# Performance work log

Measured on AMD Instinct MI355X. Metric: run time of the kernel, lower is better.

## Reference

```python
import jax, jax.numpy as jnp
import numpy as np

NB, D, H, DH, DHID = 12, 512, 8, 64, 1024  # n_blocks, d_model, n_heads, d_head, d_hidden
B, S = 2, 2048
EPS = 1e-5


def _ln(x, g, b):
    m = jnp.mean(x, axis=-1, keepdims=True)
    v = jnp.mean(jnp.square(x - m), axis=-1, keepdims=True)
    return (x - m) / jnp.sqrt(v + EPS) * g + b


def setup_inputs() -> dict:
    key = jax.random.key(0)
    ks = jax.random.split(key, 8)
    s = 0.02
    f32 = jnp.float32
    return {
        "X": jax.random.normal(ks[0], (B, S, D), f32),
        "qkv_w": jax.random.normal(ks[1], (NB, D, 3 * D), f32) * s,
        "qkv_b": jnp.zeros((NB, 3 * D), f32),
        "fc_w": jax.random.normal(ks[2], (NB, D, D), f32) * s,
        "fc_b": jnp.zeros((NB, D), f32),
        "ln1_g": jnp.ones((NB, D), f32),
        "ln1_b": jnp.zeros((NB, D), f32),
        "w1": jax.random.normal(ks[3], (NB, D, DHID), f32) * s,
        "b1": jnp.zeros((NB, DHID), f32),
        "w2": jax.random.normal(ks[4], (NB, DHID, D), f32) * s,
        "b2": jnp.zeros((NB, D), f32),
        "ln2_g": jnp.ones((NB, D), f32),
        "ln2_b": jnp.zeros((NB, D), f32),
    }


def reference(X, qkv_w, qkv_b, fc_w, fc_b, ln1_g, ln1_b, w1, b1, w2, b2, ln2_g, ln2_b):
    scale = 1.0 / np.sqrt(D)  # NOTE: original scales by 1/sqrt(d_model), not 1/sqrt(d_head)

    def body(x, p):
        qw, qb, fw, fb, g1, be1, w1_, bb1, w2_, bb2, g2, be2 = p
        b, s, _ = x.shape
        # qkv -> [b, h, s, 3*dh]; split per-head AFTER head reshape (as in chunk(dim=-1))
        ctx = (x @ qw + qb).reshape(b, s, H, 3 * DH).transpose(0, 2, 1, 3)
        q, k, v = jnp.split(ctx, 3, axis=-1)  # each [b, h, s, dh]
        attn = jax.nn.softmax(jnp.einsum('bhqd,bhkd->bhqk', q, k) * scale, axis=-1)
        o = jnp.einsum('bhqk,bhkd->bhqd', attn, v).transpose(0, 2, 1, 3).reshape(b, s, D)
        x = x + (o @ fw + fb)                      # residual + attn out proj (dropout=0)
        h = jax.nn.relu(_ln(x, g1, be1) @ w1_ + bb1)
        x = x + (h @ w2_ + bb2)                    # residual + MLP
        return _ln(x, g2, be2), None

    out, _ = jax.lax.scan(
        body, X,
        (qkv_w, qkv_b, fc_w, fc_b, ln1_g, ln1_b, w1, b1, w2, b2, ln2_g, ln2_b))
    return out
```

## Files before the change

kernel.cpp:

```cpp
#include <hip/hip_runtime.h>

typedef unsigned short ushort_t;
typedef __attribute__((ext_vector_type(8))) short bf16x8;
typedef __attribute__((ext_vector_type(4))) float f32x4;
typedef __attribute__((ext_vector_type(4))) unsigned short us4;

#define DEV __device__ __forceinline__

DEV ushort_t f2b(float f) {
    union { float f; unsigned u; } x; x.f = f;
    unsigned r = (x.u + 0x7fffu + ((x.u >> 16) & 1u)) >> 16;
    return (ushort_t)r;
}

DEV float b2f(ushort_t u) {
    union { unsigned u; float f; } x; x.u = ((unsigned)u) << 16;
    return x.f;
}

DEV unsigned cvt_pk_bf16(float lo, float hi) {
    unsigned r;
    asm("v_cvt_pk_bf16_f32 %0, %1, %2" : "=v"(r) : "v"(lo), "v"(hi));
    return r;
}

typedef void __attribute__((address_space(1)))* gp1;
typedef void __attribute__((address_space(3)))* sp3;
DEV void gload_lds16(const void* g, void* l) {
    __builtin_amdgcn_global_load_lds((gp1)g, (sp3)l, 16, 0, 0);
}

__global__ __launch_bounds__(256) void transpose_cvt(
    const float* __restrict__ in, ushort_t* __restrict__ out, int K, int N)
{
    __shared__ float tile[32][33];
    const int nb = blockIdx.z;
    const float* src = in + (size_t)nb * K * N;
    ushort_t* dst = out + (size_t)nb * K * N;
    const int n0 = blockIdx.x * 32, k0 = blockIdx.y * 32;
    const int tx = threadIdx.x & 31, ty = threadIdx.x >> 5;
#pragma unroll
    for (int i = 0; i < 32; i += 8)
        tile[ty + i][tx] = src[(size_t)(k0 + ty + i) * N + n0 + tx];
    __syncthreads();
#pragma unroll
    for (int i = 0; i < 32; i += 8)
        dst[(size_t)(n0 + ty + i) * K + k0 + tx] = f2b(tile[tx][ty + i]);
}

__global__ __launch_bounds__(256) void init_x(
    const float* __restrict__ X, float* __restrict__ xf, ushort_t* __restrict__ xb)
{
    const int i = blockIdx.x * 256 + threadIdx.x;
    const float4 v = ((const float4*)X)[i];
    ((float4*)xf)[i] = v;
    us4 o = { f2b(v.x), f2b(v.y), f2b(v.z), f2b(v.w) };
    ((us4*)xb)[i] = o;
}

enum { EPI_QKV = 0, EPI_RELUB = 2 };

template<int EPI>
__global__ __launch_bounds__(256, 2) void gemm64(
    const ushort_t* __restrict__ A, const ushort_t* __restrict__ Wt,
    const float* __restrict__ bias, ushort_t* __restrict__ Cb,
    ushort_t* __restrict__ Oq, ushort_t* __restrict__ Ok, ushort_t* __restrict__ Ov,
    int M, int N, int K, float qs)
{
    __shared__ __align__(16) ushort_t lA[2][64 * 64];
    __shared__ __align__(16) ushort_t lB[2][128 * 64];
    const int nbm = M >> 6;
    const int bm = blockIdx.x % nbm;
    const int bn = blockIdx.x / nbm;
    const int tid = threadIdx.x, lane = tid & 63, w = tid >> 6;
    const int l15 = lane & 15, l4 = lane >> 4;

    f32x4 acc[4][2];
#pragma unroll
    for (int i = 0; i < 4; i++)
#pragma unroll
        for (int j = 0; j < 2; j++) { f32x4 z = {0.f, 0.f, 0.f, 0.f}; acc[i][j] = z; }

    const int srow = tid >> 3;
    const int sch = tid & 7;
    const int swch = sch ^ (srow & 7);
    const ushort_t* Asrc0 = A  + (size_t)(bm * 64 + srow) * K + swch * 8;
    const ushort_t* Asrc1 = A  + (size_t)(bm * 64 + srow + 32) * K + swch * 8;
    const ushort_t* Bsrc0 = Wt + (size_t)(bn * 128 + srow) * K + swch * 8;
    const ushort_t* Bsrc1 = Wt + (size_t)(bn * 128 + srow + 32) * K + swch * 8;
    const ushort_t* Bsrc2 = Wt + (size_t)(bn * 128 + srow + 64) * K + swch * 8;
    const ushort_t* Bsrc3 = Wt + (size_t)(bn * 128 + srow + 96) * K + swch * 8;
    char* lAc = (char*)lA;
    char* lBc = (char*)lB;

#define GE_STAGE(buf, k0) do {                                            \
        gload_lds16(Asrc0 + (k0), lAc + (buf) * 8192  + w * 1024);        \
        gload_lds16(Asrc1 + (k0), lAc + (buf) * 8192  + 4096 + w * 1024); \
        gload_lds16(Bsrc0 + (k0), lBc + (buf) * 16384 + w * 1024);        \
        gload_lds16(Bsrc1 + (k0), lBc + (buf) * 16384 + 4096 + w * 1024); \
        gload_lds16(Bsrc2 + (k0), lBc + (buf) * 16384 + 8192 + w * 1024); \
        gload_lds16(Bsrc3 + (k0), lBc + (buf) * 16384 + 12288 + w * 1024);\
    } while (0)

    GE_STAGE(0, 0);
    __syncthreads();

    const int nIt = K >> 6;
    int cur = 0;
    for (int it = 0; it < nIt; ++it) {
        if (it + 1 < nIt) GE_STAGE(cur ^ 1, (it + 1) * 64);
#pragma unroll
        for (int ks = 0; ks < 2; ks++) {
            bf16x8 af[4], bfr[2];
#pragma unroll
            for (int i = 0; i < 4; i++) {
                const int row = i * 16 + l15;
                af[i] = *(const bf16x8*)(lAc + cur * 8192 + row * 128 +
                                         (((ks * 4 + l4) ^ (row & 7)) << 4));
            }
#pragma unroll
            for (int j = 0; j < 2; j++) {
                const int row = w * 32 + j * 16 + l15;
                bfr[j] = *(const bf16x8*)(lBc + cur * 16384 + row * 128 +
                                          (((ks * 4 + l4) ^ (row & 7)) << 4));
            }
#pragma unroll
            for (int i = 0; i < 4; i++)
#pragma unroll
                for (int j = 0; j < 2; j++)
                    acc[i][j] = __builtin_amdgcn_mfma_f32_16x16x32_bf16(af[i], bfr[j], acc[i][j], 0, 0, 0);
        }
        __syncthreads();
        cur ^= 1;
    }
#undef GE_STAGE

    const int mbase = bm * 64;
    const int nbase = bn * 128 + w * 32;
#pragma unroll
    for (int j = 0; j < 2; j++) {
        const int nf16 = nbase + j * 16;
        const float bv = bias[nf16 + l15];
        if constexpr (EPI == EPI_QKV) {
            const int head = nf16 / 192;
            const int rem = nf16 - head * 192;
            const int part = rem >> 6;
            const int dh = (rem & 63) + l15;
#pragma unroll
            for (int i = 0; i < 4; i++) {
                const int m0 = mbase + i * 16 + l4 * 4;
                const int b = m0 >> 11, s0 = m0 & 2047;
                if (part == 2) {
                    us4 pv;
#pragma unroll
                    for (int r = 0; r < 4; r++) pv[r] = f2b(acc[i][j][r] + bv);
                    *(us4*)(&Ov[((size_t)(b * 8 + head) * 64 + dh) * 2048 + s0]) = pv;
                } else if (part == 0) {
#pragma unroll
                    for (int r = 0; r < 4; r++)
                        Oq[((size_t)(b * 8 + head) * 2048 + s0 + r) * 64 + dh] =
                            f2b((acc[i][j][r] + bv) * qs);
                } else {
#pragma unroll
                    for (int r = 0; r < 4; r++)
                        Ok[((size_t)(b * 8 + head) * 2048 + s0 + r) * 64 + dh] =
                            f2b(acc[i][j][r] + bv);
                }
            }
        } else {
#pragma unroll
            for (int i = 0; i < 4; i++) {
                const int m0 = mbase + i * 16 + l4 * 4;
#pragma unroll
                for (int r = 0; r < 4; r++) {
                    const size_t idx = (size_t)(m0 + r) * N + nf16 + l15;
                    const float v = acc[i][j][r] + bv;
                    Cb[idx] = f2b(v > 0.f ? v : 0.f);
                }
            }
        }
    }
}

__global__ __launch_bounds__(256, 2) void gemm64_splitk(
    const ushort_t* __restrict__ A, const ushort_t* __restrict__ Wt,
    float* __restrict__ P0, float* __restrict__ P1, int M, int N, int K)
{
    __shared__ __align__(16) ushort_t lA[2][64 * 64];
    __shared__ __align__(16) ushort_t lB[2][128 * 64];
    const int nbm = M >> 6;
    const int nbn = N >> 7;
    int bid = blockIdx.x;
    const int bm = bid % nbm; bid /= nbm;
    const int bn = bid % nbn;
    const int kh = bid / nbn;
    const int Keff = K >> 1;
    const int kbase = kh * Keff;
    const int tid = threadIdx.x, lane = tid & 63, w = tid >> 6;
    const int l15 = lane & 15, l4 = lane >> 4;

    f32x4 acc[4][2];
#pragma unroll
    for (int i = 0; i < 4; i++)
#pragma unroll
        for (int j = 0; j < 2; j++) { f32x4 z = {0.f, 0.f, 0.f, 0.f}; acc[i][j] = z; }

    const int srow = tid >> 3;
    const int sch = tid & 7;
    const int swch = sch ^ (srow & 7);
    const ushort_t* Asrc0 = A  + (size_t)(bm * 64 + srow) * K + kbase + swch * 8;
    const ushort_t* Asrc1 = A  + (size_t)(bm * 64 + srow + 32) * K + kbase + swch * 8;
    const ushort_t* Bsrc0 = Wt + (size_t)(bn * 128 + srow) * K + kbase + swch * 8;
    const ushort_t* Bsrc1 = Wt + (size_t)(bn * 128 + srow + 32) * K + kbase + swch * 8;
    const ushort_t* Bsrc2 = Wt + (size_t)(bn * 128 + srow + 64) * K + kbase + swch * 8;
    const ushort_t* Bsrc3 = Wt + (size_t)(bn * 128 + srow + 96) * K + kbase + swch * 8;
    char* lAc = (char*)lA;
    char* lBc = (char*)lB;

#define GE_STAGE(buf, k0) do {                                            \
        gload_lds16(Asrc0 + (k0), lAc + (buf) * 8192  + w * 1024);        \
        gload_lds16(Asrc1 + (k0), lAc + (buf) * 8192  + 4096 + w * 1024); \
        gload_lds16(Bsrc0 + (k0), lBc + (buf) * 16384 + w * 1024);        \
        gload_lds16(Bsrc1 + (k0), lBc + (buf) * 16384 + 4096 + w * 1024); \
        gload_lds16(Bsrc2 + (k0), lBc + (buf) * 16384 + 8192 + w * 1024); \
        gload_lds16(Bsrc3 + (k0), lBc + (buf) * 16384 + 12288 + w * 1024);\
    } while (0)

    GE_STAGE(0, 0);
    __syncthreads();

    const int nIt = Keff >> 6;
    int cur = 0;
    for (int it = 0; it < nIt; ++it) {
        if (it + 1 < nIt) GE_STAGE(cur ^ 1, (it + 1) * 64);
#pragma unroll
        for (int ks = 0; ks < 2; ks++) {
            bf16x8 af[4], bfr[2];
#pragma unroll
            for (int i = 0; i < 4; i++) {
                const int row = i * 16 + l15;
                af[i] = *(const bf16x8*)(lAc + cur * 8192 + row * 128 +
                                         (((ks * 4 + l4) ^ (row & 7)) << 4));
            }
#pragma unroll
            for (int j = 0; j < 2; j++) {
                const int row = w * 32 + j * 16 + l15;
                bfr[j] = *(const bf16x8*)(lBc + cur * 16384 + row * 128 +
                                          (((ks * 4 + l4) ^ (row & 7)) << 4));
            }
#pragma unroll
            for (int i = 0; i < 4; i++)
#pragma unroll
                for (int j = 0; j < 2; j++)
                    acc[i][j] = __builtin_amdgcn_mfma_f32_16x16x32_bf16(af[i], bfr[j], acc[i][j], 0, 0, 0);
        }
        __syncthreads();
        cur ^= 1;
    }
#undef GE_STAGE

    float* out = kh ? P1 : P0;
    const int mbase = bm * 64;
    const int nbase = bn * 128 + w * 32;
#pragma unroll
    for (int j = 0; j < 2; j++) {
        const int nf16 = nbase + j * 16;
#pragma unroll
        for (int i = 0; i < 4; i++) {
            const int m0 = mbase + i * 16 + l4 * 4;
#pragma unroll
            for (int r = 0; r < 4; r++)
                out[(size_t)(m0 + r) * N + nf16 + l15] = acc[i][j][r];
        }
    }
}

__global__ __launch_bounds__(256, 4) void flash_attn7(
    const ushort_t* __restrict__ Q, const ushort_t* __restrict__ Kg,
    const ushort_t* __restrict__ Vg, ushort_t* __restrict__ Opart,
    float* __restrict__ lbuf)
{
    __shared__ __align__(16) ushort_t lK[2][64 * 64];
    __shared__ __align__(16) ushort_t lV[2][64 * 64];
    __shared__ __align__(16) ushort_t lP[4][32 * 64];

    const int id = blockIdx.x;
    const int rest = id >> 3;
    const int kvh = rest & 1;
    const int qt = (rest >> 1) & 15;
    const int bh = (id & 7) + ((rest >> 5) << 3);
    const int tid = threadIdx.x, lane = tid & 63, w = tid >> 6;
    const int l15 = lane & 15, l4 = lane >> 4;
    const int qrow0 = qt * 128 + w * 32;

    const ushort_t* Qb = Q + ((size_t)bh * 2048 + qrow0) * 64;
    bf16x8 qf[2][2];
#pragma unroll
    for (int qi = 0; qi < 2; qi++)
#pragma unroll
        for (int ks = 0; ks < 2; ks++)
            qf[qi][ks] = *(const bf16x8*)(Qb + (qi * 16 + l15) * 64 + ks * 32 + l4 * 8);

    const ushort_t* Kbase = Kg + (size_t)bh * 2048 * 64;
    const ushort_t* Vbase = Vg + (size_t)bh * 64 * 2048;

    const f32x4 FZ = { 0.f, 0.f, 0.f, 0.f };
    float l_run[2] = { 0.f, 0.f };
    f32x4 oacc[2][4];
#pragma unroll
    for (int qi = 0; qi < 2; qi++)
#pragma unroll
        for (int nd = 0; nd < 4; nd++) oacc[qi][nd] = FZ;

    char* lKc = (char*)lK;
    char* lVc = (char*)lV;
    char* myP = (char*)(lP[w]);

    const int srow8 = lane >> 3;
    const int sch = lane & 7;

#define FA_STAGE(buf, kt) do {                                              \
        const int row0_ = w * 16 + srow8;                                   \
        const int sc0_ = sch ^ (row0_ & 7);                                 \
        gload_lds16(Kbase + (size_t)((kt) * 64 + row0_) * 64 + sc0_ * 8,    \
                    lKc + (buf) * 8192 + w * 2048);                         \
        gload_lds16(Vbase + (size_t)row0_ * 2048 + (kt) * 64 + sc0_ * 8,    \
                    lVc + (buf) * 8192 + w * 2048);                         \
        gload_lds16(Kbase + (size_t)((kt) * 64 + row0_ + 8) * 64 + sc0_ * 8,\
                    lKc + (buf) * 8192 + w * 2048 + 1024);                  \
        gload_lds16(Vbase + (size_t)(row0_ + 8) * 2048 + (kt) * 64 + sc0_ * 8,\
                    lVc + (buf) * 8192 + w * 2048 + 1024);                  \
    } while (0)

#define FA_BODY(CUR, IT) do {                                               \
    if ((IT) < 15) FA_STAGE((CUR) ^ 1, kt0 + (IT) + 1);                     \
    f32x4 sc[2][4];                                                         \
    __builtin_amdgcn_s_setprio(1);                                          \
    _Pragma("unroll")                                                       \
    for (int nf = 0; nf < 4; nf++) {                                        \
        const int krow = nf * 16 + l15;                                     \
        const bf16x8 kf0 = *(const bf16x8*)(lKc + (CUR) * 8192 + krow * 128 + \
                                            ((l4 ^ (krow & 7)) << 4));      \
        const bf16x8 kf1 = *(const bf16x8*)(lKc + (CUR) * 8192 + krow * 128 + \
                                            (((4 + l4) ^ (krow & 7)) << 4)); \
        sc[0][nf] = __builtin_amdgcn_mfma_f32_16x16x32_bf16(kf0, qf[0][0], FZ, 0, 0, 0); \
        sc[1][nf] = __builtin_amdgcn_mfma_f32_16x16x32_bf16(kf0, qf[1][0], FZ, 0, 0, 0); \
        sc[0][nf] = __builtin_amdgcn_mfma_f32_16x16x32_bf16(kf1, qf[0][1], sc[0][nf], 0, 0, 0); \
        sc[1][nf] = __builtin_amdgcn_mfma_f32_16x16x32_bf16(kf1, qf[1][1], sc[1][nf], 0, 0, 0); \
    }                                                                       \
    __builtin_amdgcn_s_setprio(0);                                          \
    _Pragma("unroll")                                                       \
    for (int qi = 0; qi < 2; qi++) {                                        \
        float ps0 = 0.f, ps1 = 0.f;                                         \
        _Pragma("unroll")                                                   \
        for (int nf = 0; nf < 4; nf++) {                                    \
            const float p0 = exp2f(sc[qi][nf][0]);                          \
            const float p1 = exp2f(sc[qi][nf][1]);                          \
            const float p2 = exp2f(sc[qi][nf][2]);                          \
            const float p3 = exp2f(sc[qi][nf][3]);                          \
            sc[qi][nf][0] = p0; sc[qi][nf][1] = p1;                         \
            sc[qi][nf][2] = p2; sc[qi][nf][3] = p3;                         \
            ps0 += p0 + p2; ps1 += p1 + p3;                                 \
        }                                                                   \
        l_run[qi] += ps0 + ps1;                                             \
    }                                                                       \
    const int hh0 = (l15 >> 3) & 1;                                         \
    _Pragma("unroll")                                                       \
    for (int qi = 0; qi < 2; qi++) {                                        \
        char* rp = myP + (qi * 16 + l15) * 128;                             \
        const int swz = (l15 & 7) << 4;                                     \
        _Pragma("unroll")                                                   \
        for (int nf = 0; nf < 4; nf++) {                                    \
            const unsigned pw0 = cvt_pk_bf16(sc[qi][nf][0], sc[qi][nf][1]); \
            const unsigned pw1 = cvt_pk_bf16(sc[qi][nf][2], sc[qi][nf][3]); \
            const unsigned wA = hh0 ? pw1 : pw0;                            \
            const unsigned wB = hh0 ? pw0 : pw1;                            \
            const int cbase = nf * 32 + l4 * 8;                             \
            *(unsigned*)(rp + ((cbase + hh0 * 4) ^ swz)) = wA;              \
            *(unsigned*)(rp + ((cbase + (1 - hh0) * 4) ^ swz)) = wB;        \
        }                                                                   \
    }                                                                       \
    __asm__ volatile("" ::: "memory");                                     \
    bf16x8 pa[2][2];                                                        \
    _Pragma("unroll")                                                       \
    for (int qi = 0; qi < 2; qi++)                                          \
        _Pragma("unroll")                                                   \
        for (int ks = 0; ks < 2; ks++)                                      \
            pa[qi][ks] = *(const bf16x8*)(myP + (qi * 16 + l15) * 128 +     \
                                          ((ks * 64 + l4 * 16) ^ ((l15 & 7) << 4))); \
    __builtin_amdgcn_s_setprio(1);                                          \
    _Pragma("unroll")                                                       \
    for (int ks = 0; ks < 2; ks++)                                          \
        _Pragma("unroll")                                                   \
        for (int nd = 0; nd < 4; nd++) {                                    \
            const int vrow = nd * 16 + l15;                                 \
            const bf16x8 vf = *(const bf16x8*)(lVc + (CUR) * 8192 + vrow * 128 + \
                                               (((ks * 4 + l4) ^ (vrow & 7)) << 4)); \
            oacc[0][nd] = __builtin_amdgcn_mfma_f32_16x16x32_bf16(pa[0][ks], vf, oacc[0][nd], 0, 0, 0); \
            oacc[1][nd] = __builtin_amdgcn_mfma_f32_16x16x32_bf16(pa[1][ks], vf, oacc[1][nd], 0, 0, 0); \
        }                                                                   \
    __builtin_amdgcn_s_setprio(0);                                          \
    __syncthreads();                                                        \
} while (0)

    const int kt0 = kvh * 16;
    FA_STAGE(0, kt0);
    __syncthreads();

    for (int it2 = 0; it2 < 8; ++it2) {
        FA_BODY(0, it2 * 2);
        FA_BODY(1, it2 * 2 + 1);
    }
#undef FA_BODY
#undef FA_STAGE

#pragma unroll
    for (int qi = 0; qi < 2; qi++) {
        l_run[qi] += __shfl_xor(l_run[qi], 16);
        l_run[qi] += __shfl_xor(l_run[qi], 32);
    }
    ushort_t* Op = Opart + ((size_t)(kvh * 16 + bh) * 2048 + qrow0) * 64;
#pragma unroll
    for (int qi = 0; qi < 2; qi++)
#pragma unroll
        for (int r = 0; r < 4; r++)
#pragma unroll
            for (int nd = 0; nd < 4; nd++)
                Op[(size_t)(qi * 16 + l4 * 4 + r) * 64 + nd * 16 + l15] =
                    f2b(oacc[qi][nd][r]);
    if (lane < 32) {
        const int qi = lane >> 4;
        lbuf[(size_t)(kvh * 16 + bh) * 2048 + qrow0 + qi * 16 + (lane & 15)] =
            qi ? l_run[1] : l_run[0];
    }
}

__global__ __launch_bounds__(256) void combine_attn(
    const ushort_t* __restrict__ Opart, const float* __restrict__ lbuf,
    ushort_t* __restrict__ O)
{
    const int gid = blockIdx.x * 256 + threadIdx.x;
    const int d4 = (gid & 15) * 4;
    const int s = (gid >> 4) & 2047;
    const int bh = gid >> 15;
    const us4 a0 = *(const us4*)(Opart + ((size_t)bh * 2048 + s) * 64 + d4);
    const us4 a1 = *(const us4*)(Opart + ((size_t)(16 + bh) * 2048 + s) * 64 + d4);
    const float l0 = lbuf[(size_t)bh * 2048 + s];
    const float l1 = lbuf[(size_t)(16 + bh) * 2048 + s];
    const float inv = 1.f / (l0 + l1);
    us4 out;
#pragma unroll
    for (int r = 0; r < 4; r++)
        out[r] = f2b((b2f(a0[r]) + b2f(a1[r])) * inv);
    const int row = (bh >> 3) * 2048 + s;
    const int col = (bh & 7) * 64 + d4;
    *(us4*)(&O[(size_t)row * 512 + col]) = out;
}

template<int CN>
__global__ __launch_bounds__(256) void ln_fused(
    const float* __restrict__ Xf, const float* __restrict__ P0,
    const float* __restrict__ P1, const float* __restrict__ bias,
    const float* __restrict__ g, const float* __restrict__ beta,
    float* __restrict__ XfOut, ushort_t* __restrict__ Yb, float* __restrict__ Yf)
{
    const int row = blockIdx.x * 4 + (threadIdx.x >> 6);
    const int lane = threadIdx.x & 63;
    const size_t base = (size_t)row * 512;
    float4 x0 = ((const float4*)(Xf + base))[lane];
    float4 x1 = ((const float4*)(Xf + base))[lane + 64];
    const float4 a0 = ((const float4*)(P0 + base))[lane];
    const float4 a1 = ((const float4*)(P0 + base))[lane + 64];
    const float4 c0 = ((const float4*)(P1 + base))[lane];
    const float4 c1 = ((const float4*)(P1 + base))[lane + 64];
    const float4 bb0 = ((const float4*)bias)[lane];
    const float4 bb1 = ((const float4*)bias)[lane + 64];
    x0.x += a0.x + c0.x + bb0.x; x0.y += a0.y + c0.y + bb0.y;
    x0.z += a0.z + c0.z + bb0.z; x0.w += a0.w + c0.w + bb0.w;
    x1.x += a1.x + c1.x + bb1.x; x1.y += a1.y + c1.y + bb1.y;
    x1.z += a1.z + c1.z + bb1.z; x1.w += a1.w + c1.w + bb1.w;

    float s = x0.x + x0.y + x0.z + x0.w + x1.x + x1.y + x1.z + x1.w;
    float s2 = x0.x * x0.x + x0.y * x0.y + x0.z * x0.z + x0.w * x0.w
             + x1.x * x1.x + x1.y * x1.y + x1.z * x1.z + x1.w * x1.w;
#pragma unroll
    for (int m = 1; m < 64; m <<= 1) { s += __shfl_xor(s, m); s2 += __shfl_xor(s2, m); }
    const float mean = s * (1.f / 512.f);
    const float inv = rsqrtf(s2 * (1.f / 512.f) - mean * mean + 1e-5f);
    const float4 g0 = ((const float4*)g)[lane], g1 = ((const float4*)g)[lane + 64];
    const float4 b0 = ((const float4*)beta)[lane], b1 = ((const float4*)beta)[lane + 64];
    float4 y0, y1;
    y0.x = (x0.x - mean) * inv * g0.x + b0.x;
    y0.y = (x0.y - mean) * inv * g0.y + b0.y;
    y0.z = (x0.z - mean) * inv * g0.z + b0.z;
    y0.w = (x0.w - mean) * inv * g0.w + b0.w;
    y1.x = (x1.x - mean) * inv * g1.x + b1.x;
    y1.y = (x1.y - mean) * inv * g1.y + b1.y;
    y1.z = (x1.z - mean) * inv * g1.z + b1.z;
    y1.w = (x1.w - mean) * inv * g1.w + b1.w;
    if constexpr (CN == 0) {
        ((float4*)(XfOut + base))[lane] = x0;
        ((float4*)(XfOut + base))[lane + 64] = x1;
    } else {
        ((float4*)(XfOut + base))[lane] = y0;
        ((float4*)(XfOut + base))[lane + 64] = y1;
        if (Yf) {
            ((float4*)(Yf + base))[lane] = y0;
            ((float4*)(Yf + base))[lane + 64] = y1;
        }
    }
    us4 o0 = { f2b(y0.x), f2b(y0.y), f2b(y0.z), f2b(y0.w) };
    us4 o1 = { f2b(y1.x), f2b(y1.y), f2b(y1.z), f2b(y1.w) };
    ((us4*)(Yb + base))[lane] = o0;
    ((us4*)(Yb + base))[lane + 64] = o1;
}

extern "C" void kernel_launch(void* const* d_in, const int* in_sizes, int n_in,
                              void* d_out, int out_size, void* d_ws, size_t ws_size,
                              hipStream_t stream)
{
    (void)in_sizes; (void)n_in; (void)out_size; (void)ws_size;
    const float* X     = (const float*)d_in[0];
    const float* qkv_w = (const float*)d_in[1];
    const float* qkv_b = (const float*)d_in[2];
    const float* fc_w  = (const float*)d_in[3];
    const float* fc_b  = (const float*)d_in[4];
    const float* ln1_g = (const float*)d_in[5];
    const float* ln1_b = (const float*)d_in[6];
    const float* w1    = (const float*)d_in[7];
    const float* b1    = (const float*)d_in[8];
    const float* w2    = (const float*)d_in[9];
    const float* b2    = (const float*)d_in[10];
    const float* ln2_g = (const float*)d_in[11];
    const float* ln2_b = (const float*)d_in[12];

    char* ws = (char*)d_ws;
    size_t off = 0;
    auto alloc = [&](size_t bytes) -> char* {
        char* p = ws + off;
        off += (bytes + 255) & ~(size_t)255;
        return p;
    };
    ushort_t* qkvw_t = (ushort_t*)alloc(12ull * 1536 * 512 * 2);
    ushort_t* fcw_t  = (ushort_t*)alloc(12ull * 512 * 512 * 2);
    ushort_t* w1_t   = (ushort_t*)alloc(12ull * 512 * 1024 * 2);
    ushort_t* w2_t   = (ushort_t*)alloc(12ull * 1024 * 512 * 2);
    float*    xf     = (float*)   alloc(4096ull * 512 * 4);
    ushort_t* xb     = (ushort_t*)alloc(4096ull * 512 * 2);
    ushort_t* qb     = (ushort_t*)alloc(16ull * 2048 * 64 * 2);
    ushort_t* kb     = (ushort_t*)alloc(16ull * 2048 * 64 * 2);
    ushort_t* vt     = (ushort_t*)alloc(16ull * 64 * 2048 * 2);
    ushort_t* ob     = (ushort_t*)alloc(4096ull * 512 * 2);
    ushort_t* y1     = (ushort_t*)alloc(4096ull * 512 * 2);
    ushort_t* hbuf   = (ushort_t*)alloc(4096ull * 1024 * 2);
    ushort_t* opart  = (ushort_t*)alloc(32ull * 2048 * 64 * 2);
    float*    lbuf   = (float*)   alloc(32ull * 2048 * 4);
    float* pk0 = (float*)qb;
    float* pk1 = (float*)opart;

    transpose_cvt<<<dim3(48, 16, 12), 256, 0, stream>>>(qkv_w, qkvw_t, 512, 1536);
    transpose_cvt<<<dim3(16, 16, 12), 256, 0, stream>>>(fc_w, fcw_t, 512, 512);
    transpose_cvt<<<dim3(32, 16, 12), 256, 0, stream>>>(w1, w1_t, 512, 1024);
    transpose_cvt<<<dim3(16, 32, 12), 256, 0, stream>>>(w2, w2_t, 1024, 512);
    init_x<<<2048, 256, 0, stream>>>(X, xf, xb);

    const float sl2 = (float)(0.044194173824159216 * 1.4426950408889634);
    for (int nb = 0; nb < 12; nb++) {
        gemm64<EPI_QKV><<<64 * 12, 256, 0, stream>>>(
            xb, qkvw_t + (size_t)nb * 1536 * 512, qkv_b + nb * 1536,
            nullptr, qb, kb, vt, 4096, 1536, 512, sl2);
        flash_attn7<<<512, 256, 0, stream>>>(qb, kb, vt, opart, lbuf);
        combine_attn<<<2048, 256, 0, stream>>>(opart, lbuf, ob);
        gemm64_splitk<<<64 * 4 * 2, 256, 0, stream>>>(
            ob, fcw_t + (size_t)nb * 512 * 512, pk0, pk1, 4096, 512, 512);
        ln_fused<0><<<1024, 256, 0, stream>>>(
            xf, pk0, pk1, fc_b + nb * 512, ln1_g + nb * 512, ln1_b + nb * 512,
            xf, y1, nullptr);
        gemm64<EPI_RELUB><<<64 * 8, 256, 0, stream>>>(
            y1, w1_t + (size_t)nb * 1024 * 512, b1 + nb * 1024,
            hbuf, nullptr, nullptr, nullptr, 4096, 1024, 512, 1.f);
        gemm64_splitk<<<64 * 4 * 2, 256, 0, stream>>>(
            hbuf, w2_t + (size_t)nb * 1024 * 512, pk0, pk1, 4096, 512, 1024);
        ln_fused<1><<<1024, 256, 0, stream>>>(
            xf, pk0, pk1, b2 + nb * 512, ln2_g + nb * 512, ln2_b + nb * 512,
            xf, xb, nb == 11 ? (float*)d_out : nullptr);
    }
}
```

Measured before the change: 1.217 ms.

## Split attention KV into four chunks and store split-K partials as bf16

Flash attention now splits the key range into four parts instead of two, doubling the grid to 1024 blocks, halving the per-wave P scratch tile, and interleaving per-qi P writes and reads. The combine kernel sums four partials. The split-K GEMM partial outputs are stored as bf16 instead of fp32, which halves the partial traffic into the layernorm kernels and lets the partial buffers alias the q/k buffers. The bf16 partials lose precision in the residual sums, and the extra attention split adds more partial writes and combine reads.

```diff
diff --git a/kernel.cpp b/kernel.cpp
--- a/kernel.cpp
+++ b/kernel.cpp
@@ -184,7 +184,7 @@
 
 __global__ __launch_bounds__(256, 2) void gemm64_splitk(
     const ushort_t* __restrict__ A, const ushort_t* __restrict__ Wt,
-    float* __restrict__ P0, float* __restrict__ P1, int M, int N, int K)
+    ushort_t* __restrict__ P0, ushort_t* __restrict__ P1, int M, int N, int K)
 {
     __shared__ __align__(16) ushort_t lA[2][64 * 64];
     __shared__ __align__(16) ushort_t lB[2][128 * 64];
@@ -259,7 +259,7 @@
     }
 #undef GE_STAGE
 
-    float* out = kh ? P1 : P0;
+    ushort_t* out = kh ? P1 : P0;
     const int mbase = bm * 64;
     const int nbase = bn * 128 + w * 32;
 #pragma unroll
@@ -270,25 +270,25 @@
             const int m0 = mbase + i * 16 + l4 * 4;
 #pragma unroll
             for (int r = 0; r < 4; r++)
-                out[(size_t)(m0 + r) * N + nf16 + l15] = acc[i][j][r];
+                out[(size_t)(m0 + r) * N + nf16 + l15] = f2b(acc[i][j][r]);
         }
     }
 }
 
-__global__ __launch_bounds__(256, 4) void flash_attn7(
+__global__ __launch_bounds__(256, 4) void flash_attn8(
     const ushort_t* __restrict__ Q, const ushort_t* __restrict__ Kg,
     const ushort_t* __restrict__ Vg, ushort_t* __restrict__ Opart,
     float* __restrict__ lbuf)
 {
     __shared__ __align__(16) ushort_t lK[2][64 * 64];
     __shared__ __align__(16) ushort_t lV[2][64 * 64];
-    __shared__ __align__(16) ushort_t lP[4][32 * 64];
+    __shared__ __align__(16) ushort_t lP[4][16 * 64];
 
     const int id = blockIdx.x;
     const int rest = id >> 3;
-    const int kvh = rest & 1;
-    const int qt = (rest >> 1) & 15;
-    const int bh = (id & 7) + ((rest >> 5) << 3);
+    const int kvh = rest & 3;
+    const int qt = (rest >> 2) & 15;
+    const int bh = (id & 7) + ((rest >> 6) << 3);
     const int tid = threadIdx.x, lane = tid & 63, w = tid >> 6;
     const int l15 = lane & 15, l4 = lane >> 4;
     const int qrow0 = qt * 128 + w * 32;
@@ -333,7 +333,7 @@
     } while (0)
 
 #define FA_BODY(CUR, IT) do {                                               \
-    if ((IT) < 15) FA_STAGE((CUR) ^ 1, kt0 + (IT) + 1);                     \
+    if ((IT) < 7) FA_STAGE((CUR) ^ 1, kt0 + (IT) + 1);                      \
     f32x4 sc[2][4];                                                         \
     __builtin_amdgcn_s_setprio(1);                                          \
     _Pragma("unroll")                                                       \
@@ -365,9 +365,10 @@
         l_run[qi] += ps0 + ps1;                                             \
     }                                                                       \
     const int hh0 = (l15 >> 3) & 1;                                         \
+    bf16x8 pa[2][2];                                                        \
     _Pragma("unroll")                                                       \
     for (int qi = 0; qi < 2; qi++) {                                        \
-        char* rp = myP + (qi * 16 + l15) * 128;                             \
+        char* rp = myP + l15 * 128;                                         \
         const int swz = (l15 & 7) << 4;                                     \
         _Pragma("unroll")                                                   \
         for (int nf = 0; nf < 4; nf++) {                                    \
@@ -379,15 +380,13 @@
             *(unsigned*)(rp + ((cbase + hh0 * 4) ^ swz)) = wA;              \
             *(unsigned*)(rp + ((cbase + (1 - hh0) * 4) ^ swz)) = wB;        \
         }                                                                   \
-    }                                                                       \
-    __asm__ volatile("" ::: "memory");                                     \
-    bf16x8 pa[2][2];                                                        \
-    _Pragma("unroll")                                                       \
-    for (int qi = 0; qi < 2; qi++)                                          \
+        __asm__ volatile("" ::: "memory");                                 \
         _Pragma("unroll")                                                   \
         for (int ks = 0; ks < 2; ks++)                                      \
-            pa[qi][ks] = *(const bf16x8*)(myP + (qi * 16 + l15) * 128 +     \
-                                          ((ks * 64 + l4 * 16) ^ ((l15 & 7) << 4))); \
+            pa[qi][ks] = *(const bf16x8*)(myP + l15 * 128 +                 \
+                                          ((ks * 64 + l4 * 16) ^ swz));     \
+        __asm__ volatile("" ::: "memory");                                 \
+    }                                                                       \
     __builtin_amdgcn_s_setprio(1);                                          \
     _Pragma("unroll")                                                       \
     for (int ks = 0; ks < 2; ks++)                                          \
@@ -403,11 +402,11 @@
     __syncthreads();                                                        \
 } while (0)
 
-    const int kt0 = kvh * 16;
+    const int kt0 = kvh * 8;
     FA_STAGE(0, kt0);
     __syncthreads();
 
-    for (int it2 = 0; it2 < 8; ++it2) {
+    for (int it2 = 0; it2 < 4; ++it2) {
         FA_BODY(0, it2 * 2);
         FA_BODY(1, it2 * 2 + 1);
     }
@@ -443,15 +442,19 @@
     const int d4 = (gid & 15) * 4;
     const int s = (gid >> 4) & 2047;
     const int bh = gid >> 15;
-    const us4 a0 = *(const us4*)(Opart + ((size_t)bh * 2048 + s) * 64 + d4);
-    const us4 a1 = *(const us4*)(Opart + ((size_t)(16 + bh) * 2048 + s) * 64 + d4);
-    const float l0 = lbuf[(size_t)bh * 2048 + s];
-    const float l1 = lbuf[(size_t)(16 + bh) * 2048 + s];
-    const float inv = 1.f / (l0 + l1);
+    float acc[4] = { 0.f, 0.f, 0.f, 0.f };
+    float lsum = 0.f;
+#pragma unroll
+    for (int k = 0; k < 4; k++) {
+        const us4 a = *(const us4*)(Opart + ((size_t)(k * 16 + bh) * 2048 + s) * 64 + d4);
+        lsum += lbuf[(size_t)(k * 16 + bh) * 2048 + s];
+#pragma unroll
+        for (int r = 0; r < 4; r++) acc[r] += b2f(a[r]);
+    }
+    const float inv = 1.f / lsum;
     us4 out;
 #pragma unroll
-    for (int r = 0; r < 4; r++)
-        out[r] = f2b((b2f(a0[r]) + b2f(a1[r])) * inv);
+    for (int r = 0; r < 4; r++) out[r] = f2b(acc[r] * inv);
     const int row = (bh >> 3) * 2048 + s;
     const int col = (bh & 7) * 64 + d4;
     *(us4*)(&O[(size_t)row * 512 + col]) = out;
@@ -459,8 +462,8 @@
 
 template<int CN>
 __global__ __launch_bounds__(256) void ln_fused(
-    const float* __restrict__ Xf, const float* __restrict__ P0,
-    const float* __restrict__ P1, const float* __restrict__ bias,
+    const float* __restrict__ Xf, const ushort_t* __restrict__ P0,
+    const ushort_t* __restrict__ P1, const float* __restrict__ bias,
     const float* __restrict__ g, const float* __restrict__ beta,
     float* __restrict__ XfOut, ushort_t* __restrict__ Yb, float* __restrict__ Yf)
 {
@@ -469,16 +472,16 @@
     const size_t base = (size_t)row * 512;
     float4 x0 = ((const float4*)(Xf + base))[lane];
     float4 x1 = ((const float4*)(Xf + base))[lane + 64];
-    const float4 a0 = ((const float4*)(P0 + base))[lane];
-    const float4 a1 = ((const float4*)(P0 + base))[lane + 64];
-    const float4 c0 = ((const float4*)(P1 + base))[lane];
-    const float4 c1 = ((const float4*)(P1 + base))[lane + 64];
+    const us4 a0 = ((const us4*)(P0 + base))[lane];
+    const us4 a1 = ((const us4*)(P0 + base))[lane + 64];
+    const us4 c0 = ((const us4*)(P1 + base))[lane];
+    const us4 c1 = ((const us4*)(P1 + base))[lane + 64];
     const float4 bb0 = ((const float4*)bias)[lane];
     const float4 bb1 = ((const float4*)bias)[lane + 64];
-    x0.x += a0.x + c0.x + bb0.x; x0.y += a0.y + c0.y + bb0.y;
-    x0.z += a0.z + c0.z + bb0.z; x0.w += a0.w + c0.w + bb0.w;
-    x1.x += a1.x + c1.x + bb1.x; x1.y += a1.y + c1.y + bb1.y;
-    x1.z += a1.z + c1.z + bb1.z; x1.w += a1.w + c1.w + bb1.w;
+    x0.x += b2f(a0[0]) + b2f(c0[0]) + bb0.x; x0.y += b2f(a0[1]) + b2f(c0[1]) + bb0.y;
+    x0.z += b2f(a0[2]) + b2f(c0[2]) + bb0.z; x0.w += b2f(a0[3]) + b2f(c0[3]) + bb0.w;
+    x1.x += b2f(a1[0]) + b2f(c1[0]) + bb1.x; x1.y += b2f(a1[1]) + b2f(c1[1]) + bb1.y;
+    x1.z += b2f(a1[2]) + b2f(c1[2]) + bb1.z; x1.w += b2f(a1[3]) + b2f(c1[3]) + bb1.w;
 
     float s = x0.x + x0.y + x0.z + x0.w + x1.x + x1.y + x1.z + x1.w;
     float s2 = x0.x * x0.x + x0.y * x0.y + x0.z * x0.z + x0.w * x0.w
@@ -553,10 +556,10 @@
     ushort_t* ob     = (ushort_t*)alloc(4096ull * 512 * 2);
     ushort_t* y1     = (ushort_t*)alloc(4096ull * 512 * 2);
     ushort_t* hbuf   = (ushort_t*)alloc(4096ull * 1024 * 2);
-    ushort_t* opart  = (ushort_t*)alloc(32ull * 2048 * 64 * 2);
-    float*    lbuf   = (float*)   alloc(32ull * 2048 * 4);
-    float* pk0 = (float*)qb;
-    float* pk1 = (float*)opart;
+    ushort_t* opart  = (ushort_t*)alloc(64ull * 2048 * 64 * 2);
+    float*    lbuf   = (float*)   alloc(64ull * 2048 * 4);
+    ushort_t* pk0 = qb;
+    ushort_t* pk1 = kb;
 
     transpose_cvt<<<dim3(48, 16, 12), 256, 0, stream>>>(qkv_w, qkvw_t, 512, 1536);
     transpose_cvt<<<dim3(16, 16, 12), 256, 0, stream>>>(fc_w, fcw_t, 512, 512);
@@ -569,7 +572,7 @@
         gemm64<EPI_QKV><<<64 * 12, 256, 0, stream>>>(
             xb, qkvw_t + (size_t)nb * 1536 * 512, qkv_b + nb * 1536,
             nullptr, qb, kb, vt, 4096, 1536, 512, sl2);
-        flash_attn7<<<512, 256, 0, stream>>>(qb, kb, vt, opart, lbuf);
+        flash_attn8<<<1024, 256, 0, stream>>>(qb, kb, vt, opart, lbuf);
         combine_attn<<<2048, 256, 0, stream>>>(opart, lbuf, ob);
         gemm64_splitk<<<64 * 4 * 2, 256, 0, stream>>>(
             ob, fcw_t + (size_t)nb * 512 * 512, pk0, pk1, 4096, 512, 512);
```

After: 1.835 ms. +50.8%, slower.
